# Optimization experiments

Hardware: AMD Instinct MI355X
Metric: run time of the kernel (lower is better)

Reference implementation:

```python
import jax, jax.numpy as jnp
import numpy as np
from jax import lax

# ---- static config (from init_kwargs / input_specs) ----
B, NB, C, F = 16, 8192, 3, 64   # batches, points-per-batch, coord dim, feat dim
RATIO, K = 0.125, 16
M = int(RATIO * NB)


def setup_inputs() -> dict:
    key = jax.random.key(0)
    kx, kp = jax.random.split(key)
    x = jax.random.normal(kx, (B * NB, F), dtype=jnp.float32)
    pos = jax.random.normal(kp, (B * NB, C), dtype=jnp.float32)
    batch = (jnp.arange(B * NB, dtype=jnp.int32) // NB).astype(jnp.int32)
    return {"x": x, "pos": pos, "batch": batch}


def _fps_single(pos_b):
    """Sequential farthest point sampling on (NB, C), deterministic start at 0.
    Returns (M,) int32 indices into pos_b."""
    n = pos_b.shape[0]

    def step(carry, _):
        min_d2, last = carry
        d2 = jnp.sum((pos_b - pos_b[last]) ** 2, axis=-1)   # (NB,)
        min_d2 = jnp.minimum(min_d2, d2)
        nxt = jnp.argmax(min_d2).astype(jnp.int32)
        return (min_d2, nxt), last

    init = (jnp.full((n,), jnp.finfo(pos_b.dtype).max, dtype=pos_b.dtype),
            jnp.int32(0))
    _, idx = lax.scan(step, init, None, length=M)
    return idx  # (M,)


def reference(x, pos, batch):
    # batch ids are block-constant (batch[i] = i // NB), so per-batch views are
    # simple reshapes -- same semantics as torch_cluster's batched fps/knn.
    pos_b = pos.reshape(B, NB, C)

    # --- farthest point sampling per batch ---
    fps_idx = jax.vmap(_fps_single)(pos_b)                            # (B, M)
    centroids = jnp.take_along_axis(pos_b, fps_idx[..., None], axis=1)  # (B, M, C)

    # --- k-NN: squared distances centroids -> all points of same batch ---
    d2 = (jnp.sum(centroids ** 2, axis=-1)[..., None]
          - 2.0 * jnp.einsum('bmc,bnc->bmn', centroids, pos_b)
          + jnp.sum(pos_b ** 2, axis=-1)[:, None, :])                 # (B, M, NB)
    _, nn_idx = lax.top_k(-d2, K)                                     # (B, M, K)

    # gather neighbor coordinates (== pos[groups_idx[1]])
    groups = jax.vmap(lambda p, i: p[i])(pos_b, nn_idx.reshape(B, M * K))  # (B, M*K, C)

    return centroids.reshape(B * M, C), groups.reshape(B * M * K, C)
```

## Files before the change

kernel.cpp:

```cpp
#include <hip/hip_runtime.h>
#include <float.h>
#include <math.h>

#define B_   16
#define NB_  8192
#define M_   1024
#define K_   16


typedef float v2f __attribute__((ext_vector_type(2)));

#define FPS_T 256
#define PPT   32
#define NPAIR (PPT/2)
#define NWAVE (FPS_T/64)

#define KNN_T   256
#define CHUNK   1024
#define GRP     8
#define BCAP    16
#define BSTRIDE 17
#define WARM    64

#define FPS_BLOCKS B_
#define WGS_PER_B  15
#define KNN_BLOCKS (B_ * WGS_PER_B)
#define MAXSP      8

__device__ __forceinline__ void topk_insert(float d2, int pi, float val[16], int idx[16])
{
    int r = 0;
    #pragma unroll
    for (int j = 0; j < 16; ++j) r += (val[j] <= d2) ? 1 : 0;
    #pragma unroll
    for (int j = 15; j >= 1; --j) {
        bool sh = (j > r);
        val[j] = sh ? val[j-1] : val[j];
        idx[j] = sh ? idx[j-1] : idx[j];
    }
    #pragma unroll
    for (int j = 0; j < 16; ++j) {
        bool pl = (j == r);
        val[j] = pl ? d2 : val[j];
        idx[j] = pl ? pi : idx[j];
    }
}

__global__ __launch_bounds__(256, 1) void fused_kernel(
    const float* __restrict__ pos, float* __restrict__ cent,
    float* __restrict__ groups, unsigned long long* __restrict__ partials,
    unsigned int* __restrict__ progress)
{
    #pragma clang fp contract(off)
    __shared__ float4 spts[NB_];
    __shared__ unsigned long long wkey[2][NWAVE];

    const int blk = blockIdx.x;
    const int t   = threadIdx.x;

    if (blk < FPS_BLOCKS) {
        const int b = blk;
        const float* pb = pos + (size_t)b * NB_ * 3;
        float* cb = cent + (size_t)b * M_ * 3;

        {
            const float4* src = (const float4*)pb;
            for (int g = t; g < NB_/4; g += FPS_T) {
                float4 f0 = src[3*g+0], f1 = src[3*g+1], f2 = src[3*g+2];
                spts[4*g+0] = make_float4(f0.x, f0.y, f0.z, 0.0f);
                spts[4*g+1] = make_float4(f0.w, f1.x, f1.y, 0.0f);
                spts[4*g+2] = make_float4(f1.z, f1.w, f2.x, 0.0f);
                spts[4*g+3] = make_float4(f2.y, f2.z, f2.w, 0.0f);
            }
        }

        v2f px2[NPAIR], py2[NPAIR], pz2[NPAIR], md2[NPAIR];
        #pragma unroll
        for (int ga = 0; ga < NPAIR/2; ++ga) {
            const float4* s4 = (const float4*)(pb + (size_t)(t*PPT + 4*ga) * 3);
            float4 f0 = s4[0], f1 = s4[1], f2 = s4[2];
            px2[2*ga]   = (v2f){f0.x, f0.w};
            py2[2*ga]   = (v2f){f0.y, f1.x};
            pz2[2*ga]   = (v2f){f0.z, f1.y};
            px2[2*ga+1] = (v2f){f1.z, f2.y};
            py2[2*ga+1] = (v2f){f1.w, f2.z};
            pz2[2*ga+1] = (v2f){f2.x, f2.w};
            md2[2*ga]   = (v2f){FLT_MAX, FLT_MAX};
            md2[2*ga+1] = (v2f){FLT_MAX, FLT_MAX};
        }
        __syncthreads();

        float lx = pb[0], ly = pb[1], lz = pb[2];
        float c0x=0,c0y=0,c0z=0,c1x=0,c1y=0,c1z=0,c2x=0,c2y=0,c2z=0,c3x=0,c3y=0,c3z=0;

        for (int m = 0; m < M_; ++m) {
            if (t == (m >> 2)) {
                const int sl = m & 3;
                if      (sl == 0) { c0x=lx; c0y=ly; c0z=lz; }
                else if (sl == 1) { c1x=lx; c1y=ly; c1z=lz; }
                else if (sl == 2) { c2x=lx; c2y=ly; c2z=lz; }
                else              { c3x=lx; c3y=ly; c3z=lz; }
            }

            if ((m & 255) == 255) {
                const int cg = m >> 8;
                if ((t >> 6) == cg) {
                    float4* o = (float4*)(cb + (size_t)t * 12);
                    o[0] = make_float4(c0x, c0y, c0z, c1x);
                    o[1] = make_float4(c1y, c1z, c2x, c2y);
                    o[2] = make_float4(c2z, c3x, c3y, c3z);
                    if ((t & 63) == 0)
                        __hip_atomic_store(&progress[b], (unsigned)(cg + 1),
                                           __ATOMIC_RELEASE, __HIP_MEMORY_SCOPE_AGENT);
                }
            }
            if (m == M_ - 1) break;

            const v2f lxv = {lx,lx}, lyv = {ly,ly}, lzv = {lz,lz};
            v2f bmax2 = {-1.0f, -1.0f};
            #pragma unroll
            for (int jj = 0; jj < NPAIR; ++jj) {
                v2f dx = px2[jj] - lxv;
                v2f dy = py2[jj] - lyv;
                v2f dz = pz2[jj] - lzv;
                v2f d2 = (dx*dx + dy*dy) + dz*dz;
                v2f mj = __builtin_elementwise_min(md2[jj], d2);
                md2[jj] = mj;
                bmax2 = __builtin_elementwise_max(bmax2, mj);
            }
            float bm = fmaxf(bmax2.x, bmax2.y);

            float v = bm;
            {
                int vi;
                vi = __builtin_amdgcn_update_dpp(__float_as_int(v), __float_as_int(v), 0xB1,  0xF, 0xF, false);
                v = fmaxf(v, __int_as_float(vi));
                vi = __builtin_amdgcn_update_dpp(__float_as_int(v), __float_as_int(v), 0x4E,  0xF, 0xF, false);
                v = fmaxf(v, __int_as_float(vi));
                vi = __builtin_amdgcn_update_dpp(__float_as_int(v), __float_as_int(v), 0x141, 0xF, 0xF, false);
                v = fmaxf(v, __int_as_float(vi));
                vi = __builtin_amdgcn_update_dpp(__float_as_int(v), __float_as_int(v), 0x140, 0xF, 0xF, false);
                v = fmaxf(v, __int_as_float(vi));
                vi = __builtin_amdgcn_update_dpp(__float_as_int(v), __float_as_int(v), 0x142, 0xF, 0xF, false);
                v = fmaxf(v, __int_as_float(vi));
                vi = __builtin_amdgcn_update_dpp(__float_as_int(v), __float_as_int(v), 0x143, 0xF, 0xF, false);
                v = fmaxf(v, __int_as_float(vi));
            }
            const float wv = __int_as_float(__builtin_amdgcn_readlane(__float_as_int(v), 63));

            int jp = -1;
            #pragma unroll
            for (int jj = NPAIR - 1; jj >= 0; --jj) {
                if (md2[jj].y == wv) jp = 2*jj + 1;
                if (md2[jj].x == wv) jp = 2*jj;
            }
            const unsigned long long mk = __ballot(jp >= 0);
            const int wl = (int)__ffsll(mk) - 1;
            const int gi = __builtin_amdgcn_readlane(t*PPT + jp, wl);

            const int par = m & 1;
            if ((t & 63) == 0)
                wkey[par][t >> 6] = ((unsigned long long)__float_as_uint(wv) << 32) |
                                    (unsigned int)(~gi);
            __syncthreads();

            unsigned long long kk = wkey[par][0];
            #pragma unroll
            for (int w = 1; w < NWAVE; ++w) {
                const unsigned long long e = wkey[par][w];
                kk = (e > kk) ? e : kk;
            }
            const int best = (int)(~(unsigned int)kk);

            const float4 c = spts[best];
            lx = c.x; ly = c.y; lz = c.z;
        }
        return;
    }

    const int r = blk - FPS_BLOCKS;
    const int b = r / WGS_PER_B;
    const int w = r % WGS_PER_B;
    int cg, sp;
    if      (w == 0) { cg = 0; sp = 0; }
    else if (w < 3)  { cg = 1; sp = w - 1; }
    else if (w < 7)  { cg = 2; sp = w - 3; }
    else             { cg = 3; sp = w - 7; }
    const int span   = NB_ >> cg;
    const int pbase  = sp * span;
    const int direct = (cg == 0);
    const int nchunks = span / CHUNK;

    float4* kpts = spts;
    unsigned long long* sbuf = (unsigned long long*)(spts + CHUNK);

    const float* pb = pos + (size_t)b * NB_ * 3;

    {
        const float4* src = (const float4*)(pb + (size_t)pbase * 3);
        float4 f0 = src[3*t+0], f1 = src[3*t+1], f2 = src[3*t+2];
        float x0=f0.x, y0=f0.y, z0=f0.z;
        float x1=f0.w, y1=f1.x, z1=f1.y;
        float x2=f1.z, y2=f1.w, z2=f2.x;
        float x3=f2.y, y3=f2.z, z3=f2.w;
        kpts[4*t+0] = make_float4(x0, y0, z0, (x0*x0 + y0*y0) + z0*z0);
        kpts[4*t+1] = make_float4(x1, y1, z1, (x1*x1 + y1*y1) + z1*z1);
        kpts[4*t+2] = make_float4(x2, y2, z2, (x2*x2 + y2*y2) + z2*z2);
        kpts[4*t+3] = make_float4(x3, y3, z3, (x3*x3 + y3*y3) + z3*z3);
    }

    if (t == 0) {
        while (__hip_atomic_load(&progress[b], __ATOMIC_ACQUIRE,
                                 __HIP_MEMORY_SCOPE_AGENT) < (unsigned)(cg + 1))
            __builtin_amdgcn_s_sleep(64);
    }
    __syncthreads();

    const int mg = b * M_ + cg * KNN_T + t;
    const float cx = cent[(size_t)mg*3+0];
    const float cy = cent[(size_t)mg*3+1];
    const float cz = cent[(size_t)mg*3+2];
    const float cn2 = (cx*cx + cy*cy) + cz*cz;

    float val[16]; int idx[16];
    #pragma unroll
    for (int j = 0; j < 16; ++j) { val[j] = FLT_MAX; idx[j] = 0; }
    int cnt = 0;
    unsigned long long* mybuf = sbuf + t * BSTRIDE;

    for (int p = 0; p < WARM; ++p) {
        float4 q = kpts[p];
        float dot = __builtin_fmaf(cz, q.z, __builtin_fmaf(cy, q.y, cx * q.x));
        float d2 = (cn2 - 2.0f*dot) + q.w;
        if (d2 < val[15]) topk_insert(d2, pbase + p, val, idx);
    }
    float tau = val[15];

    int pstart = WARM;
    for (int c = 0; c < nchunks; ++c) {
        const int ps = pbase + c * CHUNK;

        for (int p0 = pstart; p0 < CHUNK; p0 += GRP) {
            if (__any(cnt > BCAP - GRP)) {
                int n = cnt; cnt = 0;
                for (int i = 0; i < n; ++i) {
                    unsigned long long e = mybuf[i];
                    float d = __uint_as_float((unsigned int)(e >> 32));
                    int pi  = (int)(e & 0xFFFFFFFFu);
                    if (d < val[15]) topk_insert(d, pi, val, idx);
                }
                tau = val[15];
            }
            float4 q[GRP];
            #pragma unroll
            for (int i = 0; i < GRP; ++i) q[i] = kpts[p0 + i];
            float d2v[GRP];
            #pragma unroll
            for (int i = 0; i < GRP; ++i) {
                float dot = __builtin_fmaf(cz, q[i].z,
                            __builtin_fmaf(cy, q[i].y, cx * q[i].x));
                d2v[i] = (cn2 - 2.0f*dot) + q[i].w;
            }
            #pragma unroll
            for (int i = 0; i < GRP; ++i) {
                mybuf[cnt] = ((unsigned long long)__float_as_uint(d2v[i]) << 32) |
                             (unsigned int)(ps + p0 + i);
                cnt += (d2v[i] < tau) ? 1 : 0;
            }
        }
        pstart = 0;

        if (c + 1 < nchunks) {
            __syncthreads();
            const int ns = pbase + (c + 1) * CHUNK;
            const float4* src = (const float4*)(pb + (size_t)ns * 3);
            float4 f0 = src[3*t+0], f1 = src[3*t+1], f2 = src[3*t+2];
            float x0=f0.x, y0=f0.y, z0=f0.z;
            float x1=f0.w, y1=f1.x, z1=f1.y;
            float x2=f1.z, y2=f1.w, z2=f2.x;
            float x3=f2.y, y3=f2.z, z3=f2.w;
            kpts[4*t+0] = make_float4(x0, y0, z0, (x0*x0 + y0*y0) + z0*z0);
            kpts[4*t+1] = make_float4(x1, y1, z1, (x1*x1 + y1*y1) + z1*z1);
            kpts[4*t+2] = make_float4(x2, y2, z2, (x2*x2 + y2*y2) + z2*z2);
            kpts[4*t+3] = make_float4(x3, y3, z3, (x3*x3 + y3*y3) + z3*z3);
            __syncthreads();
        }
    }
    {
        int n = cnt;
        for (int i = 0; i < n; ++i) {
            unsigned long long e = mybuf[i];
            float d = __uint_as_float((unsigned int)(e >> 32));
            int pi  = (int)(e & 0xFFFFFFFFu);
            if (d < val[15]) topk_insert(d, pi, val, idx);
        }
    }

    if (direct) {
        float* g = groups + (size_t)mg * K_ * 3;
        #pragma unroll
        for (int kq = 0; kq < 16; ++kq) {
            const float* s = pb + (size_t)idx[kq] * 3;
            g[kq*3+0] = s[0]; g[kq*3+1] = s[1]; g[kq*3+2] = s[2];
        }
        return;
    }

    const int cidx = b * 3 + (cg - 1);
    const int nsp  = 1 << cg;
    {
        unsigned long long* o = partials + (((size_t)cidx * 256 + t) * MAXSP + sp) * 16;
        #pragma unroll
        for (int kq = 0; kq < 16; ++kq)
            o[kq] = ((unsigned long long)__float_as_uint(val[kq]) << 32) | (unsigned int)idx[kq];
    }
    __threadfence();
    __syncthreads();
    unsigned int* counters = progress + 16;
    if (t == 0)
        wkey[0][0] = (unsigned long long)atomicAdd(&counters[cidx], 1u);
    __syncthreads();
    if ((unsigned)wkey[0][0] != (unsigned)(nsp - 1))
        return;

    __threadfence();
    {
        float mval[16]; int midx[16];
        #pragma unroll
        for (int j = 0; j < 16; ++j) { mval[j] = FLT_MAX; midx[j] = 0; }
        const unsigned long long* base2 = partials + (((size_t)cidx * 256 + t) * MAXSP) * 16;
        for (int s2 = 0; s2 < nsp; ++s2) {
            const unsigned long long* l = base2 + s2 * 16;
            #pragma unroll
            for (int kq = 0; kq < 16; ++kq) {
                unsigned long long e = l[kq];
                float d = __uint_as_float((unsigned int)(e >> 32));
                int pi  = (int)(e & 0xFFFFFFFFu);
                if (d < mval[15]) topk_insert(d, pi, mval, midx);
            }
        }
        float* g = groups + (size_t)mg * K_ * 3;
        #pragma unroll
        for (int kq = 0; kq < 16; ++kq) {
            const float* s = pb + (size_t)midx[kq] * 3;
            g[kq*3+0] = s[0]; g[kq*3+1] = s[1]; g[kq*3+2] = s[2];
        }
    }
}

__global__ __launch_bounds__(FPS_T, 1) void fps_kernel(const float* __restrict__ pos,
                                                       float* __restrict__ cent)
{
    #pragma clang fp contract(off)
    const int b = blockIdx.x;
    const int t = threadIdx.x;
    const float* pb = pos + (size_t)b * NB_ * 3;
    float* cb = cent + (size_t)b * M_ * 3;

    __shared__ float4 spts[NB_];
    __shared__ unsigned long long wkey[2][NWAVE];

    for (int p = t; p < NB_; p += FPS_T) {
        const float* s = pb + (size_t)p * 3;
        spts[p] = make_float4(s[0], s[1], s[2], 0.0f);
    }

    v2f px2[NPAIR], py2[NPAIR], pz2[NPAIR], md2[NPAIR];
    #pragma unroll
    for (int jj = 0; jj < NPAIR; ++jj) {
        const float* s0 = pb + (size_t)(t*PPT + 2*jj) * 3;
        px2[jj] = (v2f){s0[0], s0[3]};
        py2[jj] = (v2f){s0[1], s0[4]};
        pz2[jj] = (v2f){s0[2], s0[5]};
        md2[jj] = (v2f){FLT_MAX, FLT_MAX};
    }
    __syncthreads();

    float lx = pb[0], ly = pb[1], lz = pb[2];
    float c0x=0,c0y=0,c0z=0,c1x=0,c1y=0,c1z=0,c2x=0,c2y=0,c2z=0,c3x=0,c3y=0,c3z=0;

    for (int m = 0; m < M_; ++m) {
        if (t == (m >> 2)) {
            const int sl = m & 3;
            if      (sl == 0) { c0x=lx; c0y=ly; c0z=lz; }
            else if (sl == 1) { c1x=lx; c1y=ly; c1z=lz; }
            else if (sl == 2) { c2x=lx; c2y=ly; c2z=lz; }
            else              { c3x=lx; c3y=ly; c3z=lz; }
        }
        if (m == M_ - 1) break;

        const v2f lxv = {lx,lx}, lyv = {ly,ly}, lzv = {lz,lz};
        v2f bmax2 = {-1.0f, -1.0f};
        #pragma unroll
        for (int jj = 0; jj < NPAIR; ++jj) {
            v2f dx = px2[jj] - lxv;
            v2f dy = py2[jj] - lyv;
            v2f dz = pz2[jj] - lzv;
            v2f d2 = (dx*dx + dy*dy) + dz*dz;
            v2f mj = __builtin_elementwise_min(md2[jj], d2);
            md2[jj] = mj;
            bmax2 = __builtin_elementwise_max(bmax2, mj);
        }
        float bm = fmaxf(bmax2.x, bmax2.y);

        float v = bm;
        {
            int vi;
            vi = __builtin_amdgcn_update_dpp(__float_as_int(v), __float_as_int(v), 0xB1,  0xF, 0xF, false);
            v = fmaxf(v, __int_as_float(vi));
            vi = __builtin_amdgcn_update_dpp(__float_as_int(v), __float_as_int(v), 0x4E,  0xF, 0xF, false);
            v = fmaxf(v, __int_as_float(vi));
            vi = __builtin_amdgcn_update_dpp(__float_as_int(v), __float_as_int(v), 0x141, 0xF, 0xF, false);
            v = fmaxf(v, __int_as_float(vi));
            vi = __builtin_amdgcn_update_dpp(__float_as_int(v), __float_as_int(v), 0x140, 0xF, 0xF, false);
            v = fmaxf(v, __int_as_float(vi));
            vi = __builtin_amdgcn_update_dpp(__float_as_int(v), __float_as_int(v), 0x142, 0xF, 0xF, false);
            v = fmaxf(v, __int_as_float(vi));
            vi = __builtin_amdgcn_update_dpp(__float_as_int(v), __float_as_int(v), 0x143, 0xF, 0xF, false);
            v = fmaxf(v, __int_as_float(vi));
        }
        const float wv = __int_as_float(__builtin_amdgcn_readlane(__float_as_int(v), 63));

        int jp = -1;
        #pragma unroll
        for (int jj = NPAIR - 1; jj >= 0; --jj) {
            if (md2[jj].y == wv) jp = 2*jj + 1;
            if (md2[jj].x == wv) jp = 2*jj;
        }
        const unsigned long long mk = __ballot(jp >= 0);
        const int wl = (int)__ffsll(mk) - 1;
        const int gi = __builtin_amdgcn_readlane(t*PPT + jp, wl);

        const int par = m & 1;
        if ((t & 63) == 0)
            wkey[par][t >> 6] = ((unsigned long long)__float_as_uint(wv) << 32) |
                                (unsigned int)(~gi);
        __syncthreads();

        unsigned long long kk = wkey[par][0];
        #pragma unroll
        for (int w = 1; w < NWAVE; ++w) {
            const unsigned long long e = wkey[par][w];
            kk = (e > kk) ? e : kk;
        }
        const int best = (int)(~(unsigned int)kk);

        const float4 c = spts[best];
        lx = c.x; ly = c.y; lz = c.z;
    }

    {
        float4* o = (float4*)(cb + (size_t)t * 12);
        o[0] = make_float4(c0x, c0y, c0z, c1x);
        o[1] = make_float4(c1y, c1z, c2x, c2y);
        o[2] = make_float4(c2z, c3x, c3y, c3z);
    }
}

__global__ __launch_bounds__(KNN_T, 2) void knn_kernel(const float* __restrict__ pos,
    const float* __restrict__ cent, float* __restrict__ groups,
    unsigned long long* __restrict__ partials, int nsplit)
{
    #pragma clang fp contract(off)
    __shared__ float4 kpts[CHUNK];
    __shared__ unsigned long long sbuf[KNN_T * BSTRIDE];

    const int wg = blockIdx.x;
    const int t  = threadIdx.x;
    const int per_b = 4 * nsplit;
    const int b  = wg / per_b;
    const int r  = wg % per_b;
    const int cg = r / nsplit;
    const int sp = r % nsplit;
    const int span  = NB_ / nsplit;
    const int pbase = sp * span;
    const int nchunks = span / CHUNK;

    const float* pb = pos + (size_t)b * NB_ * 3;
    const int mg = b * M_ + cg * KNN_T + t;
    const float cx = cent[(size_t)mg*3+0];
    const float cy = cent[(size_t)mg*3+1];
    const float cz = cent[(size_t)mg*3+2];
    const float cn2 = (cx*cx + cy*cy) + cz*cz;

    float val[16]; int idx[16];
    #pragma unroll
    for (int j = 0; j < 16; ++j) { val[j] = FLT_MAX; idx[j] = 0; }
    float tau = FLT_MAX;
    int cnt = 0;
    unsigned long long* mybuf = sbuf + t * BSTRIDE;

    for (int c = 0; c < nchunks; ++c) {
        const int ps = pbase + c * CHUNK;
        __syncthreads();
        for (int p = t; p < CHUNK; p += KNN_T) {
            const float* s = pb + (size_t)(ps + p) * 3;
            float x = s[0], y = s[1], z = s[2];
            float pn2 = (x*x + y*y) + z*z;
            kpts[p] = make_float4(x, y, z, pn2);
        }
        __syncthreads();

        for (int p0 = 0; p0 < CHUNK; p0 += GRP) {
            if (__any(cnt > BCAP - GRP)) {
                int n = cnt; cnt = 0;
                for (int i = 0; i < n; ++i) {
                    unsigned long long e = mybuf[i];
                    float d = __uint_as_float((unsigned int)(e >> 32));
                    int pi  = (int)(e & 0xFFFFFFFFu);
                    if (d < val[15]) topk_insert(d, pi, val, idx);
                }
                tau = val[15];
            }
            float4 q[GRP];
            #pragma unroll
            for (int i = 0; i < GRP; ++i) q[i] = kpts[p0 + i];
            float d2v[GRP];
            #pragma unroll
            for (int i = 0; i < GRP; ++i) {
                float dot = __builtin_fmaf(cz, q[i].z,
                            __builtin_fmaf(cy, q[i].y, cx * q[i].x));
                d2v[i] = (cn2 - 2.0f*dot) + q[i].w;
            }
            #pragma unroll
            for (int i = 0; i < GRP; ++i) {
                if (d2v[i] < tau) {
                    mybuf[cnt] = ((unsigned long long)__float_as_uint(d2v[i]) << 32) |
                                 (unsigned int)(ps + p0 + i);
                    ++cnt;
                }
            }
        }
    }
    {
        int n = cnt;
        for (int i = 0; i < n; ++i) {
            unsigned long long e = mybuf[i];
            float d = __uint_as_float((unsigned int)(e >> 32));
            int pi  = (int)(e & 0xFFFFFFFFu);
            if (d < val[15]) topk_insert(d, pi, val, idx);
        }
    }

    if (nsplit > 1) {
        unsigned long long* o = partials + ((size_t)mg * nsplit + sp) * 16;
        #pragma unroll
        for (int kq = 0; kq < 16; ++kq)
            o[kq] = ((unsigned long long)__float_as_uint(val[kq]) << 32) | (unsigned int)idx[kq];
    } else {
        float* g = groups + (size_t)mg * K_ * 3;
        #pragma unroll
        for (int kq = 0; kq < 16; ++kq) {
            const float* s = pb + (size_t)idx[kq] * 3;
            g[kq*3+0] = s[0]; g[kq*3+1] = s[1]; g[kq*3+2] = s[2];
        }
    }
}

__global__ __launch_bounds__(256, 2) void knn_merge(const float* __restrict__ pos,
    const unsigned long long* __restrict__ partials, float* __restrict__ groups,
    int nsplit)
{
    const int mg = blockIdx.x * 256 + threadIdx.x;
    const int b  = mg >> 10;
    const float* pb = pos + (size_t)b * NB_ * 3;

    float val[16]; int idx[16];
    #pragma unroll
    for (int j = 0; j < 16; ++j) { val[j] = FLT_MAX; idx[j] = 0; }
    for (int sp = 0; sp < nsplit; ++sp) {
        const unsigned long long* l = partials + ((size_t)mg * nsplit + sp) * 16;
        #pragma unroll
        for (int kq = 0; kq < 16; ++kq) {
            unsigned long long e = l[kq];
            float d = __uint_as_float((unsigned int)(e >> 32));
            int pi  = (int)(e & 0xFFFFFFFFu);
            if (d < val[15]) topk_insert(d, pi, val, idx);
        }
    }
    float* g = groups + (size_t)mg * K_ * 3;
    #pragma unroll
    for (int kq = 0; kq < 16; ++kq) {
        const float* s = pb + (size_t)idx[kq] * 3;
        g[kq*3+0] = s[0]; g[kq*3+1] = s[1]; g[kq*3+2] = s[2];
    }
}

extern "C" void kernel_launch(void* const* d_in, const int* in_sizes, int n_in,
                              void* d_out, int out_size, void* d_ws, size_t ws_size,
                              hipStream_t stream)
{
    (void)in_sizes; (void)n_in; (void)out_size;
    const float* pos = (const float*)d_in[1];
    float* out    = (float*)d_out;
    float* cent   = out;
    float* groups = out + (size_t)B_ * M_ * 3;

    const size_t FLAGS = 256;
    const size_t PART  = (size_t)B_ * 768 * MAXSP * 16 * sizeof(unsigned long long);

    if (ws_size >= FLAGS + PART) {
        unsigned int* progress = (unsigned int*)d_ws;
        unsigned long long* partials = (unsigned long long*)((char*)d_ws + FLAGS);

        hipMemsetAsync(d_ws, 0, FLAGS, stream);

        fused_kernel<<<FPS_BLOCKS + KNN_BLOCKS, 256, 0, stream>>>(pos, cent, groups,
                                                                  partials, progress);
    } else {
        fps_kernel<<<B_, FPS_T, 0, stream>>>(pos, cent);
        const size_t lst = (size_t)B_ * M_ * 16 * sizeof(unsigned long long);
        int nsplit = (ws_size >= 8*lst) ? 8 : (ws_size >= 4*lst) ? 4 :
                     (ws_size >= 2*lst) ? 2 : 1;
        knn_kernel<<<B_ * 4 * nsplit, KNN_T, 0, stream>>>(pos, cent, groups,
                                                          (unsigned long long*)d_ws, nsplit);
        if (nsplit > 1)
            knn_merge<<<(B_ * M_) / 256, 256, 0, stream>>>(pos,
                (const unsigned long long*)d_ws, groups, nsplit);
    }
}
```

Before: 1.270 ms.

## Double fused kernel block size to 512 threads, splitting FPS and kNN work

The fused kernel now launches 512 threads per block. FPS blocks give each thread 16 points instead of 32, shortening the per-iteration distance/max loop but adding a wave to the cross-wave reduction. Centroids are published every 128 samples, so kNN blocks can start earlier. kNN blocks split each centroid's point span across two 256-thread halves and merge their top-16 lists through shared memory. This exposes more parallelism on the sequential FPS critical path, at the cost of extra synchronisation and merge work.

```diff
diff --git a/kernel.cpp b/kernel.cpp
--- a/kernel.cpp
+++ b/kernel.cpp
@@ -10,22 +10,29 @@
 
 typedef float v2f __attribute__((ext_vector_type(2)));
 
+#define BT     512
+#define PPTF   16
+#define NPF    (PPTF/2)
+#define NWV    (BT/64)
+#define PUB    128
+
+#define CHUNK   1024
+#define HCHUNK  512
+#define GRP     8
+#define BCAP    16
+#define BSTRIDE 17
+#define WARM    64
+
+#define FPS_BLOCKS B_
+#define WGS_PER_B  15
+#define KNN_BLOCKS (B_ * WGS_PER_B)
+#define MAXSP      8
+
 #define FPS_T 256
 #define PPT   32
 #define NPAIR (PPT/2)
 #define NWAVE (FPS_T/64)
-
-#define KNN_T   256
-#define CHUNK   1024
-#define GRP     8
-#define BCAP    16
-#define BSTRIDE 17
-#define WARM    64
-
-#define FPS_BLOCKS B_
-#define WGS_PER_B  15
-#define KNN_BLOCKS (B_ * WGS_PER_B)
-#define MAXSP      8
+#define KNN_T 256
 
 __device__ __forceinline__ void topk_insert(float d2, int pi, float val[16], int idx[16])
 {
@@ -46,14 +53,14 @@
     }
 }
 
-__global__ __launch_bounds__(256, 1) void fused_kernel(
+__global__ __launch_bounds__(BT, 1) void fused_kernel(
     const float* __restrict__ pos, float* __restrict__ cent,
     float* __restrict__ groups, unsigned long long* __restrict__ partials,
     unsigned int* __restrict__ progress)
 {
     #pragma clang fp contract(off)
     __shared__ float4 spts[NB_];
-    __shared__ unsigned long long wkey[2][NWAVE];
+    __shared__ unsigned long long wkey[2][NWV];
 
     const int blk = blockIdx.x;
     const int t   = threadIdx.x;
@@ -65,7 +72,7 @@
 
         {
             const float4* src = (const float4*)pb;
-            for (int g = t; g < NB_/4; g += FPS_T) {
+            for (int g = t; g < NB_/4; g += BT) {
                 float4 f0 = src[3*g+0], f1 = src[3*g+1], f2 = src[3*g+2];
                 spts[4*g+0] = make_float4(f0.x, f0.y, f0.z, 0.0f);
                 spts[4*g+1] = make_float4(f0.w, f1.x, f1.y, 0.0f);
@@ -74,10 +81,10 @@
             }
         }
 
-        v2f px2[NPAIR], py2[NPAIR], pz2[NPAIR], md2[NPAIR];
-        #pragma unroll
-        for (int ga = 0; ga < NPAIR/2; ++ga) {
-            const float4* s4 = (const float4*)(pb + (size_t)(t*PPT + 4*ga) * 3);
+        v2f px2[NPF], py2[NPF], pz2[NPF], md2[NPF];
+        #pragma unroll
+        for (int ga = 0; ga < NPF/2; ++ga) {
+            const float4* s4 = (const float4*)(pb + (size_t)(t*PPTF + 4*ga) * 3);
             float4 f0 = s4[0], f1 = s4[1], f2 = s4[2];
             px2[2*ga]   = (v2f){f0.x, f0.w};
             py2[2*ga]   = (v2f){f0.y, f1.x};
@@ -91,26 +98,23 @@
         __syncthreads();
 
         float lx = pb[0], ly = pb[1], lz = pb[2];
-        float c0x=0,c0y=0,c0z=0,c1x=0,c1y=0,c1z=0,c2x=0,c2y=0,c2z=0,c3x=0,c3y=0,c3z=0;
+        float c0x=0,c0y=0,c0z=0,c1x=0,c1y=0,c1z=0;
 
         for (int m = 0; m < M_; ++m) {
-            if (t == (m >> 2)) {
-                const int sl = m & 3;
-                if      (sl == 0) { c0x=lx; c0y=ly; c0z=lz; }
-                else if (sl == 1) { c1x=lx; c1y=ly; c1z=lz; }
-                else if (sl == 2) { c2x=lx; c2y=ly; c2z=lz; }
-                else              { c3x=lx; c3y=ly; c3z=lz; }
-            }
-
-            if ((m & 255) == 255) {
-                const int cg = m >> 8;
-                if ((t >> 6) == cg) {
-                    float4* o = (float4*)(cb + (size_t)t * 12);
-                    o[0] = make_float4(c0x, c0y, c0z, c1x);
-                    o[1] = make_float4(c1y, c1z, c2x, c2y);
-                    o[2] = make_float4(c2z, c3x, c3y, c3z);
+            if (t == (m >> 1)) {
+                if ((m & 1) == 0) { c0x=lx; c0y=ly; c0z=lz; }
+                else              { c1x=lx; c1y=ly; c1z=lz; }
+            }
+
+            if ((m & (PUB-1)) == (PUB-1)) {
+                const int u = m >> 7;
+                if ((t >> 6) == u) {
+                    float2* o = (float2*)(cb + (size_t)t * 6);
+                    o[0] = make_float2(c0x, c0y);
+                    o[1] = make_float2(c0z, c1x);
+                    o[2] = make_float2(c1y, c1z);
                     if ((t & 63) == 0)
-                        __hip_atomic_store(&progress[b], (unsigned)(cg + 1),
+                        __hip_atomic_store(&progress[b], (unsigned)(u + 1),
                                            __ATOMIC_RELEASE, __HIP_MEMORY_SCOPE_AGENT);
                 }
             }
@@ -119,7 +123,7 @@
             const v2f lxv = {lx,lx}, lyv = {ly,ly}, lzv = {lz,lz};
             v2f bmax2 = {-1.0f, -1.0f};
             #pragma unroll
-            for (int jj = 0; jj < NPAIR; ++jj) {
+            for (int jj = 0; jj < NPF; ++jj) {
                 v2f dx = px2[jj] - lxv;
                 v2f dy = py2[jj] - lyv;
                 v2f dz = pz2[jj] - lzv;
@@ -150,13 +154,13 @@
 
             int jp = -1;
             #pragma unroll
-            for (int jj = NPAIR - 1; jj >= 0; --jj) {
+            for (int jj = NPF - 1; jj >= 0; --jj) {
                 if (md2[jj].y == wv) jp = 2*jj + 1;
                 if (md2[jj].x == wv) jp = 2*jj;
             }
             const unsigned long long mk = __ballot(jp >= 0);
             const int wl = (int)__ffsll(mk) - 1;
-            const int gi = __builtin_amdgcn_readlane(t*PPT + jp, wl);
+            const int gi = __builtin_amdgcn_readlane(t*PPTF + jp, wl);
 
             const int par = m & 1;
             if ((t & 63) == 0)
@@ -166,7 +170,7 @@
 
             unsigned long long kk = wkey[par][0];
             #pragma unroll
-            for (int w = 1; w < NWAVE; ++w) {
+            for (int w = 1; w < NWV; ++w) {
                 const unsigned long long e = wkey[par][w];
                 kk = (e > kk) ? e : kk;
             }
@@ -189,7 +193,11 @@
     const int span   = NB_ >> cg;
     const int pbase  = sp * span;
     const int direct = (cg == 0);
-    const int nchunks = span / CHUNK;
+    const int half   = span >> 1;
+    const int iters  = span >> 10;
+    const int c      = t & 255;
+    const int h      = t >> 8;
+    const int hbase  = pbase + h * half;
 
     float4* kpts = spts;
     unsigned long long* sbuf = (unsigned long long*)(spts + CHUNK);
@@ -197,26 +205,25 @@
     const float* pb = pos + (size_t)b * NB_ * 3;
 
     {
-        const float4* src = (const float4*)(pb + (size_t)pbase * 3);
-        float4 f0 = src[3*t+0], f1 = src[3*t+1], f2 = src[3*t+2];
-        float x0=f0.x, y0=f0.y, z0=f0.z;
-        float x1=f0.w, y1=f1.x, z1=f1.y;
-        float x2=f1.z, y2=f1.w, z2=f2.x;
-        float x3=f2.y, y3=f2.z, z3=f2.w;
-        kpts[4*t+0] = make_float4(x0, y0, z0, (x0*x0 + y0*y0) + z0*z0);
-        kpts[4*t+1] = make_float4(x1, y1, z1, (x1*x1 + y1*y1) + z1*z1);
-        kpts[4*t+2] = make_float4(x2, y2, z2, (x2*x2 + y2*y2) + z2*z2);
-        kpts[4*t+3] = make_float4(x3, y3, z3, (x3*x3 + y3*y3) + z3*z3);
+        const int u = 2 * t;
+        const int gidx = (u < HCHUNK) ? (pbase + u)
+                                      : (pbase + half + (u - HCHUNK));
+        const float2* src = (const float2*)(pb + (size_t)gidx * 3);
+        float2 a = src[0], d = src[1], e = src[2];
+        float x0=a.x, y0=a.y, z0=d.x;
+        float x1=d.y, y1=e.x, z1=e.y;
+        kpts[u]   = make_float4(x0, y0, z0, (x0*x0 + y0*y0) + z0*z0);
+        kpts[u+1] = make_float4(x1, y1, z1, (x1*x1 + y1*y1) + z1*z1);
     }
 
     if (t == 0) {
         while (__hip_atomic_load(&progress[b], __ATOMIC_ACQUIRE,
-                                 __HIP_MEMORY_SCOPE_AGENT) < (unsigned)(cg + 1))
+                                 __HIP_MEMORY_SCOPE_AGENT) < (unsigned)(2*cg + 2))
             __builtin_amdgcn_s_sleep(64);
     }
     __syncthreads();
 
-    const int mg = b * M_ + cg * KNN_T + t;
+    const int mg = b * M_ + cg * 256 + c;
     const float cx = cent[(size_t)mg*3+0];
     const float cy = cent[(size_t)mg*3+1];
     const float cz = cent[(size_t)mg*3+2];
@@ -226,105 +233,121 @@
     #pragma unroll
     for (int j = 0; j < 16; ++j) { val[j] = FLT_MAX; idx[j] = 0; }
     int cnt = 0;
-    unsigned long long* mybuf = sbuf + t * BSTRIDE;
+    unsigned long long* mybuf = sbuf + (size_t)t * BSTRIDE;
 
     for (int p = 0; p < WARM; ++p) {
-        float4 q = kpts[p];
+        float4 q = kpts[HCHUNK*h + p];
         float dot = __builtin_fmaf(cz, q.z, __builtin_fmaf(cy, q.y, cx * q.x));
         float d2 = (cn2 - 2.0f*dot) + q.w;
-        if (d2 < val[15]) topk_insert(d2, pbase + p, val, idx);
+        if (d2 < val[15]) topk_insert(d2, hbase + p, val, idx);
     }
     float tau = val[15];
 
-    int pstart = WARM;
-    for (int c = 0; c < nchunks; ++c) {
-        const int ps = pbase + c * CHUNK;
-
-        for (int p0 = pstart; p0 < CHUNK; p0 += GRP) {
-            if (__any(cnt > BCAP - GRP)) {
-                int n = cnt; cnt = 0;
-                for (int i = 0; i < n; ++i) {
-                    unsigned long long e = mybuf[i];
-                    float d = __uint_as_float((unsigned int)(e >> 32));
-                    int pi  = (int)(e & 0xFFFFFFFFu);
-                    if (d < val[15]) topk_insert(d, pi, val, idx);
-                }
-                tau = val[15];
-            }
-            float4 q[GRP];
-            #pragma unroll
-            for (int i = 0; i < GRP; ++i) q[i] = kpts[p0 + i];
-            float d2v[GRP];
-            #pragma unroll
-            for (int i = 0; i < GRP; ++i) {
-                float dot = __builtin_fmaf(cz, q[i].z,
-                            __builtin_fmaf(cy, q[i].y, cx * q[i].x));
-                d2v[i] = (cn2 - 2.0f*dot) + q[i].w;
-            }
-            #pragma unroll
-            for (int i = 0; i < GRP; ++i) {
-                mybuf[cnt] = ((unsigned long long)__float_as_uint(d2v[i]) << 32) |
-                             (unsigned int)(ps + p0 + i);
-                cnt += (d2v[i] < tau) ? 1 : 0;
-            }
-        }
-        pstart = 0;
-
-        if (c + 1 < nchunks) {
-            __syncthreads();
-            const int ns = pbase + (c + 1) * CHUNK;
-            const float4* src = (const float4*)(pb + (size_t)ns * 3);
-            float4 f0 = src[3*t+0], f1 = src[3*t+1], f2 = src[3*t+2];
-            float x0=f0.x, y0=f0.y, z0=f0.z;
-            float x1=f0.w, y1=f1.x, z1=f1.y;
-            float x2=f1.z, y2=f1.w, z2=f2.x;
-            float x3=f2.y, y3=f2.z, z3=f2.w;
-            kpts[4*t+0] = make_float4(x0, y0, z0, (x0*x0 + y0*y0) + z0*z0);
-            kpts[4*t+1] = make_float4(x1, y1, z1, (x1*x1 + y1*y1) + z1*z1);
-            kpts[4*t+2] = make_float4(x2, y2, z2, (x2*x2 + y2*y2) + z2*z2);
-            kpts[4*t+3] = make_float4(x3, y3, z3, (x3*x3 + y3*y3) + z3*z3);
-            __syncthreads();
-        }
-    }
-    {
-        int n = cnt;
+    auto flushbuf = [&]() {
+        int n = cnt; cnt = 0;
         for (int i = 0; i < n; ++i) {
             unsigned long long e = mybuf[i];
             float d = __uint_as_float((unsigned int)(e >> 32));
             int pi  = (int)(e & 0xFFFFFFFFu);
             if (d < val[15]) topk_insert(d, pi, val, idx);
         }
+        tau = val[15];
+    };
+
+    for (int cix = 0; cix < iters; ++cix) {
+        const int gbase = hbase + cix * HCHUNK;
+        const int p0s = (cix == 0) ? WARM : 0;
+
+        for (int p0 = p0s; p0 < HCHUNK; p0 += GRP) {
+            if (__any(cnt > BCAP - GRP)) flushbuf();
+            float4 q[GRP];
+            #pragma unroll
+            for (int i = 0; i < GRP; ++i) q[i] = kpts[HCHUNK*h + p0 + i];
+            float d2v[GRP];
+            #pragma unroll
+            for (int i = 0; i < GRP; ++i) {
+                float dot = __builtin_fmaf(cz, q[i].z,
+                            __builtin_fmaf(cy, q[i].y, cx * q[i].x));
+                d2v[i] = (cn2 - 2.0f*dot) + q[i].w;
+            }
+            #pragma unroll
+            for (int i = 0; i < GRP; ++i) {
+                if (d2v[i] < tau) {
+                    mybuf[cnt] = ((unsigned long long)__float_as_uint(d2v[i]) << 32) |
+                                 (unsigned int)(gbase + p0 + i);
+                    ++cnt;
+                }
+            }
+        }
+
+        if (cix + 1 < iters) {
+            __syncthreads();
+            const int u = 2 * t;
+            const int nb = (cix + 1) * HCHUNK;
+            const int gidx = (u < HCHUNK) ? (pbase + nb + u)
+                                          : (pbase + half + nb + (u - HCHUNK));
+            const float2* src = (const float2*)(pb + (size_t)gidx * 3);
+            float2 a = src[0], d = src[1], e = src[2];
+            float x0=a.x, y0=a.y, z0=d.x;
+            float x1=d.y, y1=e.x, z1=e.y;
+            kpts[u]   = make_float4(x0, y0, z0, (x0*x0 + y0*y0) + z0*z0);
+            kpts[u+1] = make_float4(x1, y1, z1, (x1*x1 + y1*y1) + z1*z1);
+            __syncthreads();
+        }
+    }
+    flushbuf();
+
+    __syncthreads();
+    if (h == 1) {
+        #pragma unroll
+        for (int kq = 0; kq < 16; ++kq)
+            mybuf[kq] = ((unsigned long long)__float_as_uint(val[kq]) << 32) |
+                        (unsigned int)idx[kq];
+    }
+    __syncthreads();
+    if (h == 0) {
+        const unsigned long long* pm = sbuf + (size_t)(t + 256) * BSTRIDE;
+        #pragma unroll
+        for (int kq = 0; kq < 16; ++kq) {
+            unsigned long long e = pm[kq];
+            float d = __uint_as_float((unsigned int)(e >> 32));
+            int pi  = (int)(e & 0xFFFFFFFFu);
+            if (d < val[15]) topk_insert(d, pi, val, idx);
+        }
     }
 
     if (direct) {
-        float* g = groups + (size_t)mg * K_ * 3;
-        #pragma unroll
-        for (int kq = 0; kq < 16; ++kq) {
-            const float* s = pb + (size_t)idx[kq] * 3;
-            g[kq*3+0] = s[0]; g[kq*3+1] = s[1]; g[kq*3+2] = s[2];
+        if (h == 0) {
+            float* g = groups + (size_t)mg * K_ * 3;
+            #pragma unroll
+            for (int kq = 0; kq < 16; ++kq) {
+                const float* s = pb + (size_t)idx[kq] * 3;
+                g[kq*3+0] = s[0]; g[kq*3+1] = s[1]; g[kq*3+2] = s[2];
+            }
         }
         return;
     }
 
     const int cidx = b * 3 + (cg - 1);
     const int nsp  = 1 << cg;
-    {
-        unsigned long long* o = partials + (((size_t)cidx * 256 + t) * MAXSP + sp) * 16;
+    if (h == 0) {
+        unsigned long long* o = partials + (((size_t)cidx * 256 + c) * MAXSP + sp) * 16;
         #pragma unroll
         for (int kq = 0; kq < 16; ++kq)
             o[kq] = ((unsigned long long)__float_as_uint(val[kq]) << 32) | (unsigned int)idx[kq];
     }
-    __threadfence();
     __syncthreads();
     unsigned int* counters = progress + 16;
-    if (t == 0)
+    if (t == 0) {
+        __threadfence();
         wkey[0][0] = (unsigned long long)atomicAdd(&counters[cidx], 1u);
+    }
     __syncthreads();
     if ((unsigned)wkey[0][0] != (unsigned)(nsp - 1))
         return;
 
     __threadfence();
-    {
+    if (t < 256) {
         float mval[16]; int midx[16];
         #pragma unroll
         for (int j = 0; j < 16; ++j) { mval[j] = FLT_MAX; midx[j] = 0; }
@@ -339,7 +362,8 @@
                 if (d < mval[15]) topk_insert(d, pi, mval, midx);
             }
         }
-        float* g = groups + (size_t)mg * K_ * 3;
+        const int mg2 = b * M_ + cg * 256 + t;
+        float* g = groups + (size_t)mg2 * K_ * 3;
         #pragma unroll
         for (int kq = 0; kq < 16; ++kq) {
             const float* s = pb + (size_t)midx[kq] * 3;
@@ -605,8 +629,8 @@
 
         hipMemsetAsync(d_ws, 0, FLAGS, stream);
 
-        fused_kernel<<<FPS_BLOCKS + KNN_BLOCKS, 256, 0, stream>>>(pos, cent, groups,
-                                                                  partials, progress);
+        fused_kernel<<<FPS_BLOCKS + KNN_BLOCKS, BT, 0, stream>>>(pos, cent, groups,
+                                                                 partials, progress);
     } else {
         fps_kernel<<<B_, FPS_T, 0, stream>>>(pos, cent);
         const size_t lst = (size_t)B_ * M_ * 16 * sizeof(unsigned long long);
```

After: 1.398 ms. +10.1%, slower.
